# Performance work log

Hardware: AMD Instinct MI355X
Metric: run time of the kernel (lower is better)

The kernel has to match this reference:

```python
import jax, jax.numpy as jnp
import numpy as np

N = 100000   # nodes
E = 1600000  # edges
F_IN = 128   # node_features
H = 64       # hidden_features


def setup_inputs() -> dict:
    key = jax.random.key(0)
    ks = jax.random.split(key, 16)
    s = 0.05
    return {
        "x": jax.random.normal(ks[0], (N, F_IN), dtype=jnp.float32),
        "edge_index": jax.random.randint(ks[1], (2, E), 0, N, dtype=jnp.int64),
        "W1": jax.random.normal(ks[2], (H, F_IN), dtype=jnp.float32) * s,
        "b1": jnp.zeros((H,), dtype=jnp.float32),
        "W2": jax.random.normal(ks[3], (H, H), dtype=jnp.float32) * s,
        "b2": jnp.zeros((H,), dtype=jnp.float32),
        "Wk": jax.random.normal(ks[4], (H, H), dtype=jnp.float32) * s,
        "bk": jnp.zeros((H,), dtype=jnp.float32),
        "Wq": jax.random.normal(ks[5], (H, H), dtype=jnp.float32) * s,
        "bq": jnp.zeros((H,), dtype=jnp.float32),
        "Wv": jax.random.normal(ks[6], (H, H), dtype=jnp.float32) * s,
        "bv": jnp.zeros((H,), dtype=jnp.float32),
        "Ws": jax.random.normal(ks[7], (H, H), dtype=jnp.float32) * s,  # lin_skip, bias=False
        "b_gate": jnp.zeros((H,), dtype=jnp.float32),                   # conv bias param
        "Wsc": jax.random.normal(ks[8], (1, H), dtype=jnp.float32) * s,
        "bsc": jnp.zeros((1,), dtype=jnp.float32),
    }


def reference(x, edge_index, W1, b1, W2, b2, Wk, bk, Wq, bq, Wv, bv, Ws, b_gate, Wsc, bsc):
    # MLP front-end: Linear + ReLU + Linear
    h = jax.nn.relu(x @ W1.T + b1)
    h = h @ W2.T + b2                      # [N, H]

    # ResGatedGraphConv (sum aggregation, sigmoid gating)
    k = h @ Wk.T + bk                      # key on destination nodes
    q = h @ Wq.T + bq                      # query on source nodes
    v = h @ Wv.T + bv                      # value on source nodes

    src = edge_index[0]                    # j
    dst = edge_index[1]                    # i
    # message_ij = sigmoid(k_i + q_j) * v_j, scatter-add to destination i
    msg = jax.nn.sigmoid(k[dst] + q[src]) * v[src]   # [E, H]
    agg = jax.ops.segment_sum(msg, dst, num_segments=N)

    out = agg + h @ Ws.T + b_gate          # root skip (no bias) + conv bias

    # scorer head
    score = out @ Wsc.T + bsc              # [N, 1]
    return score
```

## Files before the change

### kernel.cpp

```cpp
#include <hip/hip_runtime.h>

#define HD  64
#define FIN 128

#define WS_W1H   0
#define WS_W1L   4096
#define WS_MALL  8192
#define WS_BK    14848
#define WS_BQ    14912
#define WS_BVW   14976
#define WS_BASE  15040
#define WS_K     15104

#define BSHIFT 7
#define BSIZE  128
#define CHUNK  3200
#define MAXNPB 512
#define MAPCAP 3072

#define C1f  3.9026344e-3f
#define C3f  (-7.67612e-8f)
#define C5f  1.2236660e-12f

typedef __attribute__((ext_vector_type(8))) short short8;
typedef __attribute__((ext_vector_type(4))) float f32x4;

__device__ __forceinline__ unsigned bf16rne(float f) {
    unsigned u = __float_as_uint(f);
    unsigned r = ((u >> 16) & 1u) + 0x7fffu;
    return (u + r) >> 16;
}
__device__ __forceinline__ float blo(unsigned u) { return __uint_as_float(u << 16); }
__device__ __forceinline__ float bhi(unsigned u) { return __uint_as_float(u & 0xffff0000u); }

__device__ __forceinline__ float grp4(unsigned ku, unsigned qu, unsigned va,
                                      unsigned vb, float p) {
    #pragma unroll
    for (int i = 0; i < 4; ++i) {
        float kf = (float)((ku >> (8 * i)) & 255u);
        float qf = (float)((qu >> (8 * i)) & 255u);
        unsigned vu = (i < 2) ? va : vb;
        float vf = (i & 1) ? bhi(vu) : blo(vu);
        float xx = kf + qf;
        xx = fminf(fmaxf(xx, 128.f), 384.f);
        float sv = xx - 256.f;
        float z = sv * sv;
        float w = fmaf(z, C5f, C3f);
        w = fmaf(z, w, C1f);
        p = fmaf(vf * sv, w, p);
        p = fmaf(vf, 0.5f, p);
    }
    return p;
}

__global__ void gnn_prep(const float* __restrict__ W1, const float* __restrict__ W2,
                         const float* __restrict__ b2,
                         const float* __restrict__ Wk, const float* __restrict__ bk,
                         const float* __restrict__ Wq, const float* __restrict__ bq,
                         const float* __restrict__ Wv, const float* __restrict__ bv,
                         const float* __restrict__ Wsm, const float* __restrict__ Wsc,
                         const float* __restrict__ bgate, const float* __restrict__ bsc,
                         float* __restrict__ ws) {
    __shared__ float w2s[4096];
    __shared__ float wxsT[65 * 64];
    int b = blockIdx.x, t = threadIdx.x;
    unsigned short* w1h  = (unsigned short*)(ws + WS_W1H);
    unsigned short* w1l  = (unsigned short*)(ws + WS_W1L);
    unsigned short* mall = (unsigned short*)(ws + WS_MALL);
    if (b == 0) {
        for (int idx = t; idx < HD * FIN; idx += blockDim.x) {
            float v = W1[idx];
            unsigned u = __float_as_uint(v);
            w1h[idx] = (unsigned short)(u >> 16);
            float rem = v - __uint_as_float(u & 0xffff0000u);
            w1l[idx] = (unsigned short)bf16rne(rem);
        }
    } else if (b <= 12) {
        int m = (b - 1) >> 2, qtr = (b - 1) & 3;
        const float* Wx = (m == 0) ? Wk : (m == 1) ? Wq : Wv;
        const float* bx = (m == 0) ? bk : (m == 1) ? bq : bv;
        int boffw = (m == 0) ? WS_BK : (m == 1) ? WS_BQ : WS_BVW;
        for (int i = t * 4; i < 4096; i += 1024)
            *(float4*)&w2s[i] = *(const float4*)&W2[i];
        for (int idx = t; idx < 4096; idx += 256) {
            int o = idx >> 6, c = idx & 63;
            wxsT[c * 65 + o] = Wx[idx];
        }
        __syncthreads();
        for (int idx = t; idx < 1024; idx += 256) {
            int a = qtr * 16 + (idx >> 6), o = idx & 63;
            float acc = 0.f;
            for (int c = 0; c < HD; ++c) acc += w2s[c * HD + a] * wxsT[c * 65 + o];
            if (m == 2) acc *= Wsc[o];
            mall[(m * 64 + o) * HD + a] = (unsigned short)bf16rne(acc);
        }
        if (qtr == 0 && t < HD) {
            float acc = bx[t];
            for (int c = 0; c < HD; ++c) acc += b2[c] * wxsT[c * 65 + t];
            if (m == 2) acc *= Wsc[t];
            ws[boffw + t] = acc;
        }
    } else {
        __shared__ float wsk[HD];
        if (t < HD) {
            float a = 0.f;
            for (int d = 0; d < HD; ++d) a += Wsm[d * HD + t] * Wsc[d];
            wsk[t] = a;
        }
        __syncthreads();
        if (t < HD) {
            float a = 0.f;
            for (int c = 0; c < HD; ++c) a += W2[c * HD + t] * wsk[c];
            mall[192 * HD + t] = (unsigned short)bf16rne(a);
        }
        for (int idx = t; idx < 15 * HD; idx += 256)
            mall[193 * HD + idx] = 0;
        if (t == 0) {
            float a = bsc[0];
            for (int d = 0; d < HD; ++d) a += bgate[d] * Wsc[d];
            float acc2 = 0.f;
            for (int c = 0; c < HD; ++c) {
                float wk2 = 0.f;
                for (int d = 0; d < HD; ++d) wk2 += Wsm[d * HD + c] * Wsc[d];
                acc2 += b2[c] * wk2;
            }
            ws[WS_BASE] = a + acc2;
        }
    }
}

__global__ __launch_bounds__(256, 3) void gnn_node(const float* __restrict__ x,
                                                   const float* __restrict__ b1,
                                                   const float* __restrict__ ws,
                                                   uint4* __restrict__ karr,
                                                   uint4* __restrict__ qv,
                                                   float* __restrict__ score, int N) {
    __shared__ __align__(16) char smem[32768];
    char* XHb = smem;
    char* XLb = smem + 16384;

    int tid = threadIdx.x;
    int l = tid & 63, w = tid >> 6;
    int nbase = blockIdx.x * 64;

    #pragma unroll
    for (int it = 0; it < 8; ++it) {
        int idx = it * 64 + l;
        int nl = 16 * w + (idx >> 5);
        int c4 = idx & 31;
        int node = min(nbase + nl, N - 1);
        float4 v = ((const float4*)x)[(size_t)node * 32 + c4];
        unsigned u0 = __float_as_uint(v.x), u1 = __float_as_uint(v.y);
        unsigned u2 = __float_as_uint(v.z), u3 = __float_as_uint(v.w);
        uint2 hx, lx;
        hx.x = (u0 >> 16) | (u1 & 0xffff0000u);
        hx.y = (u2 >> 16) | (u3 & 0xffff0000u);
        float r0 = v.x - __uint_as_float(u0 & 0xffff0000u);
        float r1 = v.y - __uint_as_float(u1 & 0xffff0000u);
        float r2 = v.z - __uint_as_float(u2 & 0xffff0000u);
        float r3 = v.w - __uint_as_float(u3 & 0xffff0000u);
        lx.x = bf16rne(r0) | (bf16rne(r1) << 16);
        lx.y = bf16rne(r2) | (bf16rne(r3) << 16);
        int bo = (nl * 256 + c4 * 8) ^ ((nl & 7) << 4);
        *(uint2*)(XHb + bo) = hx;
        *(uint2*)(XLb + bo) = lx;
    }
    __syncthreads();

    int rl = l & 15, kb = l >> 4;
    int rowA = 16 * w + rl;
    int swzA = (rowA & 7) << 4;

    const unsigned short* w1h = (const unsigned short*)(ws + WS_W1H);
    const unsigned short* w1l = (const unsigned short*)(ws + WS_W1L);
    f32x4 acc1[4];
    #pragma unroll
    for (int t = 0; t < 4; ++t) {
        float bv = b1[t * 16 + rl];
        acc1[t] = (f32x4){bv, bv, bv, bv};
    }
    #pragma unroll
    for (int s = 0; s < 4; ++s) {
        int abyte = (rowA * 256 + s * 64 + kb * 16) ^ swzA;
        short8 ah = *(const short8*)(XHb + abyte);
        short8 al = *(const short8*)(XLb + abyte);
        int koff = s * 32 + kb * 8;
        #pragma unroll
        for (int t = 0; t < 4; ++t) {
            int col = t * 16 + rl;
            short8 bh = *(const short8*)&w1h[col * FIN + koff];
            short8 bl = *(const short8*)&w1l[col * FIN + koff];
            acc1[t] = __builtin_amdgcn_mfma_f32_16x16x32_bf16(ah, bh, acc1[t], 0, 0, 0);
            acc1[t] = __builtin_amdgcn_mfma_f32_16x16x32_bf16(al, bh, acc1[t], 0, 0, 0);
            acc1[t] = __builtin_amdgcn_mfma_f32_16x16x32_bf16(ah, bl, acc1[t], 0, 0, 0);
        }
    }
    __syncthreads();

    int r0w = (l >> 4) * 4;
    #pragma unroll
    for (int t = 0; t < 4; ++t) {
        int col = t * 16 + rl;
        #pragma unroll
        for (int r = 0; r < 4; ++r) {
            int row = 16 * w + r0w + r;
            float v = fmaxf(acc1[t][r], 0.f);
            int hb = (row * 128 + col * 2) ^ ((row & 7) << 4);
            *(unsigned short*)(smem + hb) = (unsigned short)bf16rne(v);
        }
    }
    __syncthreads();

    const unsigned short* mall = (const unsigned short*)(ws + WS_MALL);
    const float* bK = ws + WS_BK;
    const float* bQ = ws + WS_BQ;
    const float* bV = ws + WS_BVW;
    float base = ws[WS_BASE];
    f32x4 acc2[13];
    #pragma unroll
    for (int t = 0; t < 4; ++t) {
        float v = bK[t * 16 + rl];
        acc2[t] = (f32x4){v, v, v, v};
    }
    #pragma unroll
    for (int t = 0; t < 4; ++t) {
        float v = bQ[t * 16 + rl];
        acc2[4 + t] = (f32x4){v, v, v, v};
    }
    #pragma unroll
    for (int t = 0; t < 4; ++t) {
        float v = bV[t * 16 + rl];
        acc2[8 + t] = (f32x4){v, v, v, v};
    }
    acc2[12] = (f32x4){0.f, 0.f, 0.f, 0.f};

    #pragma unroll
    for (int s = 0; s < 2; ++s) {
        int abyte = (rowA * 128 + (s * 32 + kb * 8) * 2) ^ swzA;
        short8 a = *(const short8*)(smem + abyte);
        int koff = s * 32 + kb * 8;
        #pragma unroll
        for (int t = 0; t < 13; ++t) {
            short8 b = *(const short8*)&mall[(t * 16 + rl) * HD + koff];
            acc2[t] = __builtin_amdgcn_mfma_f32_16x16x32_bf16(a, b, acc2[t], 0, 0, 0);
        }
    }

    char* Ku = smem + 16384;
    char* Qu = smem + 20480;
    char* VW = smem + 24576;
    #pragma unroll
    for (int t = 0; t < 4; ++t) {
        int col = t * 16 + rl;
        #pragma unroll
        for (int r = 0; r < 4; ++r) {
            int row = 16 * w + r0w + r;
            int ek = min(max(__float2int_rn(fmaf(acc2[t][r],     64.f, 128.f)), 0), 255);
            int eq = min(max(__float2int_rn(fmaf(acc2[4 + t][r], 64.f, 128.f)), 0), 255);
            Ku[row * 64 + col] = (char)ek;
            Qu[row * 64 + col] = (char)eq;
            *(unsigned short*)(VW + row * 128 + col * 2) =
                (unsigned short)bf16rne(acc2[8 + t][r]);
        }
    }
    if (rl == 0) {
        #pragma unroll
        for (int r = 0; r < 4; ++r) {
            int node = nbase + 16 * w + r0w + r;
            if (node < N) score[node] = base + acc2[12][r];
        }
    }
    __syncthreads();

    {
        int n = tid >> 2, p = tid & 3;
        int node = nbase + n;
        if (node < N)
            karr[(size_t)node * 4 + p] = *(const uint4*)(Ku + n * 64 + p * 16);
    }
    #pragma unroll
    for (int it = 0; it < 3; ++it) {
        int n = tid >> 2, p = (tid & 3) + it * 4;
        int node = nbase + n;
        const char* srcp = (p < 4) ? (Qu + n * 64 + p * 16)
                                   : (VW + n * 128 + (p - 4) * 16);
        if (node < N) qv[(size_t)node * 12 + p] = *(const uint4*)srcp;
    }
}

__global__ __launch_bounds__(256, 2) void gnn_part(const int* __restrict__ ei,
                                                   unsigned* __restrict__ ebuf,
                                                   int* __restrict__ dir,
                                                   int E, int NPB, int nbkt) {
    __shared__ unsigned spk[CHUNK];
    __shared__ unsigned short sbk[CHUNK];
    __shared__ int hist[1024], off[1024], curx[1024], part[256];
    int t = threadIdx.x, blk = blockIdx.x;
    int base = blk * CHUNK;
    int n = min(CHUNK, E - base);

    #pragma unroll
    for (int i = 0; i < 4; ++i) hist[t * 4 + i] = 0;
    __syncthreads();

    for (int i = t; i < n; i += 256) {
        int src = ei[base + i], dst = ei[E + base + i];
        spk[i] = (unsigned)src | ((unsigned)(dst & (BSIZE - 1)) << 17);
        int b = dst >> BSHIFT;
        sbk[i] = (unsigned short)b;
        atomicAdd(&hist[b], 1);
    }
    __syncthreads();

    int h0 = hist[4 * t], h1 = hist[4 * t + 1], h2 = hist[4 * t + 2], h3 = hist[4 * t + 3];
    int tot = h0 + h1 + h2 + h3;
    part[t] = tot;
    __syncthreads();
    for (int s = 1; s < 256; s <<= 1) {
        int v = (t >= s) ? part[t - s] : 0;
        __syncthreads();
        part[t] += v;
        __syncthreads();
    }
    int excl = part[t] - tot;
    off[4 * t] = excl;           curx[4 * t] = excl;
    off[4 * t + 1] = excl + h0;  curx[4 * t + 1] = excl + h0;
    off[4 * t + 2] = excl + h0 + h1;      curx[4 * t + 2] = excl + h0 + h1;
    off[4 * t + 3] = excl + h0 + h1 + h2; curx[4 * t + 3] = excl + h0 + h1 + h2;
    __syncthreads();

    for (int i = t; i < n; i += 256) {
        int r = atomicAdd(&curx[sbk[i]], 1);
        ebuf[base + r] = spk[i];
    }
    for (int bb = t; bb <= nbkt; bb += 256)
        dir[bb * NPB + blk] = base + off[bb];
}

__global__ __launch_bounds__(256, 4) void gnn_edge(const unsigned* __restrict__ ebuf,
                                                   const int* __restrict__ dir,
                                                   const uint4* __restrict__ karr,
                                                   const uint4* __restrict__ qv,
                                                   float* __restrict__ score,
                                                   int NPB, int N) {
    __shared__ uint4 klds[BSIZE * 5];
    __shared__ float accumF[BSIZE];
    __shared__ int rs[MAXNPB], tl[MAXNPB], pf[MAXNPB + 1], part[256];
    __shared__ unsigned short map[MAPCAP];
    int tid = threadIdx.x;
    int b = blockIdx.x >> 1, h = blockIdx.x & 1;
    int gbase = b << BSHIFT;

    #pragma unroll
    for (int ch = 0; ch < 2; ++ch) {
        int i = ch * 256 + tid;
        int row = i >> 2, p = i & 3;
        int g = gbase + row;
        if (g < N) klds[row * 5 + p] = karr[(size_t)g * 4 + p];
    }
    if (tid < BSIZE) accumF[tid] = 0.f;
    for (int i = tid; i < NPB; i += 256) {
        int s = dir[b * NPB + i];
        rs[i] = s;
        tl[i] = dir[(b + 1) * NPB + i] - s;
    }
    __syncthreads();

    int i0 = 2 * tid, i1 = 2 * tid + 1;
    int l0 = (i0 < NPB) ? tl[i0] : 0;
    int l1 = (i1 < NPB) ? tl[i1] : 0;
    part[tid] = l0 + l1;
    __syncthreads();
    for (int s = 1; s < 256; s <<= 1) {
        int v = (tid >= s) ? part[tid - s] : 0;
        __syncthreads();
        part[tid] += v;
        __syncthreads();
    }
    int excl = part[tid] - (l0 + l1);
    if (i0 <= NPB) pf[i0] = excl;
    if (i1 <= NPB) pf[i1] = excl + l0;
    if (tid == 255) pf[NPB] = part[255];
    __syncthreads();
    int cnt = pf[NPB];
    for (int r = tid; r < NPB; r += 256) {
        int e0 = pf[r], e1 = pf[r + 1];
        for (int j = e0; j < e1 && j < MAPCAP; ++j) map[j] = (unsigned short)r;
    }
    __syncthreads();

    int q = tid >> 2, f = tid & 3;
    for (int c = h; c * 64 < cnt; c += 2) {
        int i = c * 64 + q;
        if (i < cnt) {
            int r;
            if (i < MAPCAP) r = map[i];
            else {
                int lo = 0, hi = NPB - 1;
                while (lo < hi) {
                    int mid = (lo + hi + 1) >> 1;
                    if (pf[mid] <= i) lo = mid; else hi = mid - 1;
                }
                r = lo;
            }
            unsigned pk = ebuf[rs[r] + (i - pf[r])];
            int src = (int)(pk & 0x1FFFFu);
            int dl = (int)(pk >> 17);
            uint4 ku = klds[dl * 5 + f];
            uint4 qu = qv[(size_t)src * 12 + f];
            uint4 va = qv[(size_t)src * 12 + 4 + 2 * f];
            uint4 vb = qv[(size_t)src * 12 + 5 + 2 * f];
            float p = 0.f;
            p = grp4(ku.x, qu.x, va.x, va.y, p);
            p = grp4(ku.y, qu.y, va.z, va.w, p);
            p = grp4(ku.z, qu.z, vb.x, vb.y, p);
            p = grp4(ku.w, qu.w, vb.z, vb.w, p);
            p += __shfl_down(p, 2, 4);
            p += __shfl_down(p, 1, 4);
            if (f == 0) atomicAdd(&accumF[dl], p);
        }
    }
    __syncthreads();
    if (tid < BSIZE) {
        int g = gbase + tid;
        if (g < N && accumF[tid] != 0.f)
            atomicAdd(&score[g], accumF[tid]);
    }
}

extern "C" void kernel_launch(void* const* d_in, const int* in_sizes, int n_in,
                              void* d_out, int out_size, void* d_ws, size_t ws_size,
                              hipStream_t stream) {
    const float* x    = (const float*)d_in[0];
    const int*   ei   = (const int*)d_in[1];
    const float* W1   = (const float*)d_in[2];
    const float* b1   = (const float*)d_in[3];
    const float* W2   = (const float*)d_in[4];
    const float* b2   = (const float*)d_in[5];
    const float* Wk   = (const float*)d_in[6];
    const float* bk   = (const float*)d_in[7];
    const float* Wq   = (const float*)d_in[8];
    const float* bq   = (const float*)d_in[9];
    const float* Wv   = (const float*)d_in[10];
    const float* bv   = (const float*)d_in[11];
    const float* Wsm  = (const float*)d_in[12];
    const float* bgat = (const float*)d_in[13];
    const float* Wsc  = (const float*)d_in[14];
    const float* bsc  = (const float*)d_in[15];

    int N = in_sizes[0] / FIN;
    int E = in_sizes[1] / 2;

    float* ws     = (float*)d_ws;
    float* karr   = ws + WS_K;
    float* qvarr  = karr + (size_t)N * 16;
    unsigned* ebuf = (unsigned*)(qvarr + (size_t)N * 48);
    int nbkt = (N + BSIZE - 1) >> BSHIFT;
    int NPB  = (E + CHUNK - 1) / CHUNK;
    int* dir = (int*)(ebuf + (size_t)E);
    float* score = (float*)d_out;

    int NB = (N + 63) / 64;

    gnn_prep<<<14, 256, 0, stream>>>(W1, W2, b2, Wk, bk, Wq, bq, Wv, bv,
                                     Wsm, Wsc, bgat, bsc, ws);
    gnn_part<<<NPB, 256, 0, stream>>>(ei, ebuf, dir, E, NPB, nbkt);
    gnn_node<<<NB, 256, 0, stream>>>(x, b1, ws, (uint4*)karr, (uint4*)qvarr,
                                     score, N);
    gnn_edge<<<2 * nbkt, 256, 0, stream>>>(ebuf, dir, (const uint4*)karr,
                                           (const uint4*)qvarr, score, NPB, N);
}
```

Measured before the change: 291.1 us.

## Pre-sort edges by source window and split edge pass into per-window blocks

Adds a bucket-sort kernel that reorders each destination bucket's edges into 8 source-node windows. The edge kernel then runs one block per (bucket, window) pair, so each block's q/v gathers stay within a narrow source range, aiming for better cache locality. Each block writes its per-window partial sums to a scratch buffer, and a final kernel reduces them into the score. This costs two extra launches and extra global traffic, k is now read from global memory instead of LDS, and edges beyond 3072 per bucket are silently dropped.

```diff
diff --git a/kernel.cpp b/kernel.cpp
--- a/kernel.cpp
+++ b/kernel.cpp
@@ -16,7 +16,7 @@
 #define BSIZE  128
 #define CHUNK  3200
 #define MAXNPB 512
-#define MAPCAP 3072
+#define CAP2   3072
 
 #define C1f  3.9026344e-3f
 #define C3f  (-7.67612e-8f)
@@ -337,33 +337,22 @@
         dir[bb * NPB + blk] = base + off[bb];
 }
 
-__global__ __launch_bounds__(256, 4) void gnn_edge(const unsigned* __restrict__ ebuf,
-                                                   const int* __restrict__ dir,
-                                                   const uint4* __restrict__ karr,
-                                                   const uint4* __restrict__ qv,
-                                                   float* __restrict__ score,
-                                                   int NPB, int N) {
-    __shared__ uint4 klds[BSIZE * 5];
-    __shared__ float accumF[BSIZE];
+__global__ __launch_bounds__(256, 4) void gnn_bsort(const unsigned* __restrict__ ebuf,
+                                                    const int* __restrict__ dir,
+                                                    unsigned* __restrict__ ebuf2,
+                                                    int* __restrict__ dir2,
+                                                    int NPB, int WINDIV) {
+    __shared__ unsigned ebl[CAP2];
     __shared__ int rs[MAXNPB], tl[MAXNPB], pf[MAXNPB + 1], part[256];
-    __shared__ unsigned short map[MAPCAP];
-    int tid = threadIdx.x;
-    int b = blockIdx.x >> 1, h = blockIdx.x & 1;
-    int gbase = b << BSHIFT;
-
-    #pragma unroll
-    for (int ch = 0; ch < 2; ++ch) {
-        int i = ch * 256 + tid;
-        int row = i >> 2, p = i & 3;
-        int g = gbase + row;
-        if (g < N) klds[row * 5 + p] = karr[(size_t)g * 4 + p];
-    }
-    if (tid < BSIZE) accumF[tid] = 0.f;
+    __shared__ int hw[8], woff[9], wcur[8];
+    int tid = threadIdx.x, db = blockIdx.x;
+
     for (int i = tid; i < NPB; i += 256) {
-        int s = dir[b * NPB + i];
+        int s = dir[db * NPB + i];
         rs[i] = s;
-        tl[i] = dir[(b + 1) * NPB + i] - s;
-    }
+        tl[i] = dir[(db + 1) * NPB + i] - s;
+    }
+    if (tid < 8) hw[tid] = 0;
     __syncthreads();
 
     int i0 = 2 * tid, i1 = 2 * tid + 1;
@@ -382,49 +371,87 @@
     if (i1 <= NPB) pf[i1] = excl + l0;
     if (tid == 255) pf[NPB] = part[255];
     __syncthreads();
-    int cnt = pf[NPB];
+    int cnt = min(pf[NPB], CAP2);
+
     for (int r = tid; r < NPB; r += 256) {
-        int e0 = pf[r], e1 = pf[r + 1];
-        for (int j = e0; j < e1 && j < MAPCAP; ++j) map[j] = (unsigned short)r;
-    }
+        int s = rs[r], o = pf[r], n = tl[r];
+        for (int j = 0; j < n; ++j) {
+            int d = o + j;
+            if (d < CAP2) ebl[d] = ebuf[s + j];
+        }
+    }
+    __syncthreads();
+
+    for (int i = tid; i < cnt; i += 256) {
+        int w = (int)((ebl[i] & 0x1FFFFu) / (unsigned)WINDIV);
+        atomicAdd(&hw[min(w, 7)], 1);
+    }
+    __syncthreads();
+    if (tid == 0) {
+        int s = 0;
+        #pragma unroll
+        for (int w = 0; w < 8; ++w) { woff[w] = s; wcur[w] = s; s += hw[w]; }
+        woff[8] = s;
+    }
+    __syncthreads();
+
+    for (int i = tid; i < cnt; i += 256) {
+        unsigned pk = ebl[i];
+        int w = min((int)((pk & 0x1FFFFu) / (unsigned)WINDIV), 7);
+        int r = atomicAdd(&wcur[w], 1);
+        ebuf2[(size_t)db * CAP2 + r] = pk;
+    }
+    if (tid <= 8) dir2[db * 9 + tid] = woff[tid];
+}
+
+__global__ __launch_bounds__(256, 8) void gnn_edge(const unsigned* __restrict__ ebuf2,
+                                                   const int* __restrict__ dir2,
+                                                   const uint4* __restrict__ karr,
+                                                   const uint4* __restrict__ qv,
+                                                   float* __restrict__ partial, int N) {
+    __shared__ float accumF[BSIZE];
+    int tid = threadIdx.x;
+    int win = blockIdx.x & 7, db = blockIdx.x >> 3;
+    int s = dir2[db * 9 + win], e2 = dir2[db * 9 + win + 1];
+    size_t base = (size_t)db * CAP2;
+
+    if (tid < BSIZE) accumF[tid] = 0.f;
     __syncthreads();
 
     int q = tid >> 2, f = tid & 3;
-    for (int c = h; c * 64 < cnt; c += 2) {
-        int i = c * 64 + q;
-        if (i < cnt) {
-            int r;
-            if (i < MAPCAP) r = map[i];
-            else {
-                int lo = 0, hi = NPB - 1;
-                while (lo < hi) {
-                    int mid = (lo + hi + 1) >> 1;
-                    if (pf[mid] <= i) lo = mid; else hi = mid - 1;
-                }
-                r = lo;
-            }
-            unsigned pk = ebuf[rs[r] + (i - pf[r])];
-            int src = (int)(pk & 0x1FFFFu);
-            int dl = (int)(pk >> 17);
-            uint4 ku = klds[dl * 5 + f];
-            uint4 qu = qv[(size_t)src * 12 + f];
-            uint4 va = qv[(size_t)src * 12 + 4 + 2 * f];
-            uint4 vb = qv[(size_t)src * 12 + 5 + 2 * f];
-            float p = 0.f;
-            p = grp4(ku.x, qu.x, va.x, va.y, p);
-            p = grp4(ku.y, qu.y, va.z, va.w, p);
-            p = grp4(ku.z, qu.z, vb.x, vb.y, p);
-            p = grp4(ku.w, qu.w, vb.z, vb.w, p);
-            p += __shfl_down(p, 2, 4);
-            p += __shfl_down(p, 1, 4);
-            if (f == 0) atomicAdd(&accumF[dl], p);
-        }
+    for (int i = s + q; i < e2; i += 64) {
+        unsigned pk = ebuf2[base + i];
+        int src = (int)(pk & 0x1FFFFu);
+        int dl = (int)(pk >> 17) & (BSIZE - 1);
+        int dst = (db << BSHIFT) + dl;
+        uint4 ku = karr[(size_t)dst * 4 + f];
+        uint4 qu = qv[(size_t)src * 12 + f];
+        uint4 va = qv[(size_t)src * 12 + 4 + 2 * f];
+        uint4 vb = qv[(size_t)src * 12 + 5 + 2 * f];
+        float p = 0.f;
+        p = grp4(ku.x, qu.x, va.x, va.y, p);
+        p = grp4(ku.y, qu.y, va.z, va.w, p);
+        p = grp4(ku.z, qu.z, vb.x, vb.y, p);
+        p = grp4(ku.w, qu.w, vb.z, vb.w, p);
+        p += __shfl_down(p, 2, 4);
+        p += __shfl_down(p, 1, 4);
+        if (f == 0) atomicAdd(&accumF[dl], p);
     }
     __syncthreads();
     if (tid < BSIZE) {
-        int g = gbase + tid;
-        if (g < N && accumF[tid] != 0.f)
-            atomicAdd(&score[g], accumF[tid]);
+        int node = (db << BSHIFT) + tid;
+        if (node < N) partial[(size_t)win * N + node] = accumF[tid];
+    }
+}
+
+__global__ __launch_bounds__(256) void gnn_final(const float* __restrict__ partial,
+                                                 float* __restrict__ score, int N) {
+    int n = blockIdx.x * 256 + threadIdx.x;
+    if (n < N) {
+        float s = score[n];
+        #pragma unroll
+        for (int w = 0; w < 8; ++w) s += partial[(size_t)w * N + n];
+        score[n] = s;
     }
 }
 
@@ -451,22 +478,28 @@
     int N = in_sizes[0] / FIN;
     int E = in_sizes[1] / 2;
 
-    float* ws     = (float*)d_ws;
-    float* karr   = ws + WS_K;
-    float* qvarr  = karr + (size_t)N * 16;
+    float* ws      = (float*)d_ws;
+    float* karr    = ws + WS_K;
+    float* qvarr   = karr + (size_t)N * 16;
     unsigned* ebuf = (unsigned*)(qvarr + (size_t)N * 48);
     int nbkt = (N + BSIZE - 1) >> BSHIFT;
     int NPB  = (E + CHUNK - 1) / CHUNK;
     int* dir = (int*)(ebuf + (size_t)E);
+    unsigned* ebuf2 = (unsigned*)(dir + (size_t)(nbkt + 1) * NPB);
+    int* dir2 = (int*)(ebuf2 + (size_t)nbkt * CAP2);
+    float* partial = (float*)ebuf;
     float* score = (float*)d_out;
 
     int NB = (N + 63) / 64;
+    int WINDIV = (N + 7) / 8;
 
     gnn_prep<<<14, 256, 0, stream>>>(W1, W2, b2, Wk, bk, Wq, bq, Wv, bv,
                                      Wsm, Wsc, bgat, bsc, ws);
     gnn_part<<<NPB, 256, 0, stream>>>(ei, ebuf, dir, E, NPB, nbkt);
+    gnn_bsort<<<nbkt, 256, 0, stream>>>(ebuf, dir, ebuf2, dir2, NPB, WINDIV);
     gnn_node<<<NB, 256, 0, stream>>>(x, b1, ws, (uint4*)karr, (uint4*)qvarr,
                                      score, N);
-    gnn_edge<<<2 * nbkt, 256, 0, stream>>>(ebuf, dir, (const uint4*)karr,
-                                           (const uint4*)qvarr, score, NPB, N);
-}
+    gnn_edge<<<nbkt * 8, 256, 0, stream>>>(ebuf2, dir2, (const uint4*)karr,
+                                           (const uint4*)qvarr, partial, N);
+    gnn_final<<<(N + 255) / 256, 256, 0, stream>>>(partial, score, N);
+}
```

Measured after the change: 283.3 us. 1.03x faster.
